# Kernel optimization log

Hardware: AMD Instinct MI355X
Metric: run time of the kernel (lower is better)

Reference implementation:

```python
import jax, jax.numpy as jnp
import numpy as np

T, B, D, H, O = 512, 64, 512, 1024, 512

def _xavier(key, shape):
    fan_out, fan_in = shape
    limit = np.sqrt(6.0 / (fan_in + fan_out))
    return jax.random.uniform(key, shape, jnp.float32, -limit, limit)

def setup_inputs() -> dict:
    key = jax.random.key(0)
    ks = jax.random.split(key, 10)
    x = jax.random.normal(ks[0], (T, B, D), jnp.float32)
    # Gate order: i, f, o, c (stacked along first axis for a fused 4H projection;
    # math identical to 8 separate Linears in the torch module, biases init to 0
    # but we randomize them slightly for a non-trivial reference).
    Wx = jnp.concatenate([_xavier(ks[1 + g], (H, D)) for g in range(4)], axis=0)  # [4H, D]
    Wh = jnp.concatenate([_xavier(ks[5 + g], (H, H)) for g in range(4)], axis=0)  # [4H, H]
    bx = jnp.zeros((4 * H,), jnp.float32)
    bh = jnp.zeros((4 * H,), jnp.float32)
    Why = _xavier(ks[9], (O, H))
    bhy = jnp.zeros((O,), jnp.float32)
    return {"x": x, "Wx": Wx, "bx": bx, "Wh": Wh, "bh": bh, "Why": Why, "bhy": bhy}

def reference(x, Wx, bx, Wh, bh, Why, bhy):
    Hd = Wh.shape[1]
    Bd = x.shape[1]
    # Precompute all input-path projections in one batched GEMM: [T, B, 4H]
    xp = jnp.einsum('tbd,gd->tbg', x, Wx) + bx + bh

    def step(carry, xp_t):
        h, c = carry
        gates = xp_t + h @ Wh.T  # [B, 4H]
        i_t = jax.nn.sigmoid(gates[:, 0 * Hd:1 * Hd])
        f_t = jax.nn.sigmoid(gates[:, 1 * Hd:2 * Hd])
        o_t = jax.nn.sigmoid(gates[:, 2 * Hd:3 * Hd])
        c_tilde = jnp.tanh(gates[:, 3 * Hd:4 * Hd])
        c = f_t * c + i_t * c_tilde
        h = o_t * jnp.tanh(c)
        return (h, c), None

    h0 = jnp.zeros((Bd, Hd), x.dtype)
    c0 = jnp.zeros((Bd, Hd), x.dtype)
    (h, c), _ = jax.lax.scan(step, (h0, c0), xp)
    return h @ Why.T + bhy  # [B, O]
```

## Files before the change

### kernel.cpp

```cpp
#include <hip/hip_runtime.h>
#include <hip/hip_bf16.h>
#include <math.h>

constexpr int T = 512;
constexpr int B = 64;
constexpr int D = 512;
constexpr int H = 1024;
constexpr int O = 512;
constexpr int GROUPS = 2;
constexpr int BG   = B / GROUPS;
constexpr int GBLK = 128;
constexpr int COLS = 32;
constexpr int KCH  = (D + H) / 8;

typedef __attribute__((ext_vector_type(8))) __bf16 bf16x8;
typedef __attribute__((ext_vector_type(4))) float  floatx4;

struct GBar {
    unsigned arr[GBLK];
};

__global__ __launch_bounds__(256) void convert_w(
    const float* __restrict__ Wx, const float* __restrict__ Wh,
    __bf16* __restrict__ Wc)
{
    const int id = blockIdx.x * 256 + threadIdx.x;
    if (id >= GBLK * KCH * COLS) return;
    const int nl     = id & 31;
    const int kchunk = (id >> 5) % KCH;
    const int strip  = id / (KCH * COLS);
    const int s  = nl >> 4;
    const int jl = (nl >> 2) & 3;
    const int g  = nl & 3;
    const int j  = strip * 8 + 2 * jl + s;
    const int k0 = kchunk * 8;
    const float* src = (k0 < D) ? &Wx[(size_t)(g * H + j) * D + k0]
                                : &Wh[(size_t)(g * H + j) * H + (k0 - D)];
    const float4 a = *(const float4*)src;
    const float4 b = *(const float4*)(src + 4);
    __bf16 t8[8] = {(__bf16)a.x,(__bf16)a.y,(__bf16)a.z,(__bf16)a.w,
                    (__bf16)b.x,(__bf16)b.y,(__bf16)b.z,(__bf16)b.w};
    *(uint4*)&Wc[(size_t)id * 8] = *(uint4*)t8;
}

__global__ __launch_bounds__(256) void make_bias(
    const float* __restrict__ bx, const float* __restrict__ bh,
    float* __restrict__ bias)
{
    const int n = blockIdx.x * 256 + threadIdx.x;
    if (n < 4 * H) {
        const int gbn = n >> 5, nl = n & 31;
        const int s  = nl >> 4;
        const int jl = (nl >> 2) & 3;
        const int g  = nl & 3;
        const int j  = gbn * 8 + 2 * jl + s;
        bias[n] = bx[g * H + j] + bh[g * H + j];
    }
}

__global__ __launch_bounds__(128, 1) void lstm_persistent(
    const float* __restrict__ x,
    const __bf16* __restrict__ Wc,
    const float* __restrict__ bias,
    __bf16* __restrict__ hbufs,
    float* __restrict__ hfin,
    GBar* bars)
{
    __shared__ __attribute__((aligned(16))) __bf16 wlds[KCH * COLS * 8];

    const int tid   = threadIdx.x;
    const int wid   = tid >> 6;
    const int lane  = tid & 63;
    const int cm    = lane & 15;
    const int q     = lane >> 4;
    const int group = blockIdx.x >> 7;
    const int gb    = blockIdx.x & 127;
    const int n0    = gb * COLS;
    GBar* bar = bars + group;
    __bf16* hb0 = hbufs + (size_t)group * 2 * BG * H;
    __bf16* hb1 = hb0 + BG * H;

    {
        const uint4* wsrc = (const uint4*)(Wc + (size_t)gb * KCH * COLS * 8);
        uint4* wdst = (uint4*)wlds;
        for (int i = tid; i < KCH * COLS; i += 128) wdst[i] = wsrc[i];
    }
    const int p4 = cm & 3;
    const int jl = cm >> 2;
    const int row_l = wid * 16 + q * 4 + p4;
    const float4 bias0q = *(const float4*)&bias[n0 + jl * 4];
    const float4 bias1q = *(const float4*)&bias[n0 + 16 + jl * 4];
    float c0 = 0.f, c1 = 0.f;
    __syncthreads();

    const int grow = group * BG + wid * 16 + cm;
    const float* xrow = x + (size_t)grow * D + q * 8;
    const int    hoff = (wid * 16 + cm) * H + q * 8;
    const __bf16* wl  = wlds + (q * 32 + cm) * 8;
    const unsigned* fa = bar->arr + (lane & 31);

    floatx4 acc[2][2];
    float4  xcur[16][2];

    auto loadx = [&](int tt) {
        const float* xr = xrow + (size_t)tt * (B * D);
        #pragma unroll
        for (int s = 0; s < 16; ++s) {
            xcur[s][0] = *(const float4*)(xr + s * 32);
            xcur[s][1] = *(const float4*)(xr + s * 32 + 4);
        }
    };
    auto xmfma = [&]() {
        acc[0][0] = (floatx4){0,0,0,0}; acc[0][1] = (floatx4){0,0,0,0};
        acc[1][0] = (floatx4){0,0,0,0}; acc[1][1] = (floatx4){0,0,0,0};
        #pragma unroll
        for (int s = 0; s < 16; ++s) {
            const float4 a0 = xcur[s][0], a1 = xcur[s][1];
            const bf16x8 af = {(__bf16)a0.x,(__bf16)a0.y,(__bf16)a0.z,(__bf16)a0.w,
                               (__bf16)a1.x,(__bf16)a1.y,(__bf16)a1.z,(__bf16)a1.w};
            const bf16x8 b0 = *(const bf16x8*)(wl + s * 1024);
            const bf16x8 b1 = *(const bf16x8*)(wl + s * 1024 + 128);
            acc[0][s & 1] = __builtin_amdgcn_mfma_f32_16x16x32_bf16(af, b0, acc[0][s & 1], 0, 0, 0);
            acc[1][s & 1] = __builtin_amdgcn_mfma_f32_16x16x32_bf16(af, b1, acc[1][s & 1], 0, 0, 0);
        }
    };

    auto quadT = [&](float v[4]) {
        float w0 = __shfl_xor(v[1], 1), w1 = __shfl_xor(v[0], 1);
        float w2 = __shfl_xor(v[3], 1), w3 = __shfl_xor(v[2], 1);
        if (p4 & 1) { v[0] = w0; v[2] = w2; } else { v[1] = w1; v[3] = w3; }
        w0 = __shfl_xor(v[2], 2); w1 = __shfl_xor(v[3], 2);
        w2 = __shfl_xor(v[0], 2); w3 = __shfl_xor(v[1], 2);
        if (p4 & 2) { v[0] = w0; v[1] = w1; } else { v[2] = w2; v[3] = w3; }
    };

    loadx(0);
    xmfma();

    for (int t = 0; t < T; ++t) {
        const __bf16* hcur = (t & 1) ? hb1 : hb0;
        __bf16*       hnxt = (t & 1) ? hb0 : hb1;

        {
            const __bf16* hbase = hcur + hoff;
            uint4 hv[32];
            unsigned ftmp;
            asm volatile(
                "1: global_load_dword %[f], %[fa], off sc0 sc1\n\t"
                "s_waitcnt vmcnt(0)\n\t"
                "v_cmp_gt_i32 vcc, %[tt], %[f]\n\t"
                "s_cbranch_vccnz 1b\n\t"
                "global_load_dwordx4 %[h0], %[hb], off sc0 sc1\n\t"
                "global_load_dwordx4 %[h1], %[hb], off offset:64 sc0 sc1\n\t"
                "global_load_dwordx4 %[h2], %[hb], off offset:128 sc0 sc1\n\t"
                "global_load_dwordx4 %[h3], %[hb], off offset:192 sc0 sc1\n\t"
                "global_load_dwordx4 %[h4], %[hb], off offset:256 sc0 sc1\n\t"
                "global_load_dwordx4 %[h5], %[hb], off offset:320 sc0 sc1\n\t"
                "global_load_dwordx4 %[h6], %[hb], off offset:384 sc0 sc1\n\t"
                "global_load_dwordx4 %[h7], %[hb], off offset:448 sc0 sc1\n\t"
                "1: global_load_dword %[f], %[fa], off offset:128 sc0 sc1\n\t"
                "s_waitcnt vmcnt(0)\n\t"
                "v_cmp_gt_i32 vcc, %[tt], %[f]\n\t"
                "s_cbranch_vccnz 1b\n\t"
                "global_load_dwordx4 %[h8], %[hb], off offset:512 sc0 sc1\n\t"
                "global_load_dwordx4 %[h9], %[hb], off offset:576 sc0 sc1\n\t"
                "global_load_dwordx4 %[h10], %[hb], off offset:640 sc0 sc1\n\t"
                "global_load_dwordx4 %[h11], %[hb], off offset:704 sc0 sc1\n\t"
                "global_load_dwordx4 %[h12], %[hb], off offset:768 sc0 sc1\n\t"
                "global_load_dwordx4 %[h13], %[hb], off offset:832 sc0 sc1\n\t"
                "global_load_dwordx4 %[h14], %[hb], off offset:896 sc0 sc1\n\t"
                "global_load_dwordx4 %[h15], %[hb], off offset:960 sc0 sc1\n\t"
                "1: global_load_dword %[f], %[fa], off offset:256 sc0 sc1\n\t"
                "s_waitcnt vmcnt(0)\n\t"
                "v_cmp_gt_i32 vcc, %[tt], %[f]\n\t"
                "s_cbranch_vccnz 1b\n\t"
                "global_load_dwordx4 %[h16], %[hb], off offset:1024 sc0 sc1\n\t"
                "global_load_dwordx4 %[h17], %[hb], off offset:1088 sc0 sc1\n\t"
                "global_load_dwordx4 %[h18], %[hb], off offset:1152 sc0 sc1\n\t"
                "global_load_dwordx4 %[h19], %[hb], off offset:1216 sc0 sc1\n\t"
                "global_load_dwordx4 %[h20], %[hb], off offset:1280 sc0 sc1\n\t"
                "global_load_dwordx4 %[h21], %[hb], off offset:1344 sc0 sc1\n\t"
                "global_load_dwordx4 %[h22], %[hb], off offset:1408 sc0 sc1\n\t"
                "global_load_dwordx4 %[h23], %[hb], off offset:1472 sc0 sc1\n\t"
                "1: global_load_dword %[f], %[fa], off offset:384 sc0 sc1\n\t"
                "s_waitcnt vmcnt(0)\n\t"
                "v_cmp_gt_i32 vcc, %[tt], %[f]\n\t"
                "s_cbranch_vccnz 1b\n\t"
                "global_load_dwordx4 %[h24], %[hb], off offset:1536 sc0 sc1\n\t"
                "global_load_dwordx4 %[h25], %[hb], off offset:1600 sc0 sc1\n\t"
                "global_load_dwordx4 %[h26], %[hb], off offset:1664 sc0 sc1\n\t"
                "global_load_dwordx4 %[h27], %[hb], off offset:1728 sc0 sc1\n\t"
                "global_load_dwordx4 %[h28], %[hb], off offset:1792 sc0 sc1\n\t"
                "global_load_dwordx4 %[h29], %[hb], off offset:1856 sc0 sc1\n\t"
                "global_load_dwordx4 %[h30], %[hb], off offset:1920 sc0 sc1\n\t"
                "global_load_dwordx4 %[h31], %[hb], off offset:1984 sc0 sc1\n\t"
                "s_waitcnt vmcnt(0)"
                : [h0]"=&v"(hv[0]),  [h1]"=&v"(hv[1]),  [h2]"=&v"(hv[2]),  [h3]"=&v"(hv[3]),
                  [h4]"=&v"(hv[4]),  [h5]"=&v"(hv[5]),  [h6]"=&v"(hv[6]),  [h7]"=&v"(hv[7]),
                  [h8]"=&v"(hv[8]),  [h9]"=&v"(hv[9]),  [h10]"=&v"(hv[10]), [h11]"=&v"(hv[11]),
                  [h12]"=&v"(hv[12]), [h13]"=&v"(hv[13]), [h14]"=&v"(hv[14]), [h15]"=&v"(hv[15]),
                  [h16]"=&v"(hv[16]), [h17]"=&v"(hv[17]), [h18]"=&v"(hv[18]), [h19]"=&v"(hv[19]),
                  [h20]"=&v"(hv[20]), [h21]"=&v"(hv[21]), [h22]"=&v"(hv[22]), [h23]"=&v"(hv[23]),
                  [h24]"=&v"(hv[24]), [h25]"=&v"(hv[25]), [h26]"=&v"(hv[26]), [h27]"=&v"(hv[27]),
                  [h28]"=&v"(hv[28]), [h29]"=&v"(hv[29]), [h30]"=&v"(hv[30]), [h31]"=&v"(hv[31]),
                  [f]"=&v"(ftmp)
                : [hb]"v"(hbase), [fa]"v"(fa), [tt]"v"(t)
                : "memory", "vcc");
            #pragma unroll
            for (int sg = 0; sg < 32; ++sg) {
                union { uint4 u; bf16x8 v; } hf; hf.u = hv[sg];
                const bf16x8 b0 = *(const bf16x8*)(wl + 16384 + sg * 1024);
                const bf16x8 b1 = *(const bf16x8*)(wl + 16384 + sg * 1024 + 128);
                acc[0][sg & 1] = __builtin_amdgcn_mfma_f32_16x16x32_bf16(hf.v, b0, acc[0][sg & 1], 0, 0, 0);
                acc[1][sg & 1] = __builtin_amdgcn_mfma_f32_16x16x32_bf16(hf.v, b1, acc[1][sg & 1], 0, 0, 0);
            }
        }
        const floatx4 av0 = acc[0][0] + acc[0][1];
        const floatx4 av1 = acc[1][0] + acc[1][1];

        float g0v[4] = {av0.x, av0.y, av0.z, av0.w};
        float g1v[4] = {av1.x, av1.y, av1.z, av1.w};
        quadT(g0v);
        quadT(g1v);

        if (t + 1 < T) loadx(t + 1);

        const float i0 = 1.f / (1.f + expf(-(g0v[0] + bias0q.x)));
        const float f0 = 1.f / (1.f + expf(-(g0v[1] + bias0q.y)));
        const float o0 = 1.f / (1.f + expf(-(g0v[2] + bias0q.z)));
        const float t0 = tanhf(g0v[3] + bias0q.w);
        const float i1 = 1.f / (1.f + expf(-(g1v[0] + bias1q.x)));
        const float f1 = 1.f / (1.f + expf(-(g1v[1] + bias1q.y)));
        const float o1 = 1.f / (1.f + expf(-(g1v[2] + bias1q.z)));
        const float t1 = tanhf(g1v[3] + bias1q.w);
        c0 = f0 * c0 + i0 * t0;
        c1 = f1 * c1 + i1 * t1;
        const float hv0 = o0 * tanhf(c0);
        const float hv1 = o1 * tanhf(c1);
        const int j0 = gb * 8 + 2 * jl;
        const int hi = row_l * H + j0;
        union { __bf16 h2[2]; unsigned u; } hp;
        hp.h2[0] = (__bf16)hv0; hp.h2[1] = (__bf16)hv1;
        __hip_atomic_store((unsigned*)&hnxt[hi], hp.u, __ATOMIC_RELAXED,
                           __HIP_MEMORY_SCOPE_AGENT);
        if (t == T - 1) {
            const int gr = group * BG + row_l;
            hfin[gr * H + j0]     = hv0;
            hfin[gr * H + j0 + 1] = hv1;
        }

        __syncthreads();

        if (tid == 0)
            __hip_atomic_store(&bar->arr[gb], (unsigned)(t + 1),
                               __ATOMIC_RELAXED, __HIP_MEMORY_SCOPE_AGENT);

        if (t + 1 < T) xmfma();
    }
}

__global__ __launch_bounds__(256) void out_gemm(
    const float* __restrict__ h, const float* __restrict__ Why,
    const float* __restrict__ bhy, float* __restrict__ out)
{
    const int idx = blockIdx.x * 256 + threadIdx.x;
    if (idx >= B * O) return;
    const int b = idx / O;
    const int o = idx % O;
    const float4* hv = (const float4*)&h[(size_t)b * H];
    const float4* wv = (const float4*)&Why[(size_t)o * H];
    float s = 0.f;
    #pragma unroll 4
    for (int k = 0; k < H / 4; ++k) {
        const float4 a = hv[k];
        const float4 w = wv[k];
        s += a.x * w.x + a.y * w.y + a.z * w.z + a.w * w.w;
    }
    out[idx] = s + bhy[o];
}

extern "C" void kernel_launch(void* const* d_in, const int* in_sizes, int n_in,
                              void* d_out, int out_size, void* d_ws, size_t ws_size,
                              hipStream_t stream) {
    const float* x   = (const float*)d_in[0];
    const float* Wx  = (const float*)d_in[1];
    const float* bx  = (const float*)d_in[2];
    const float* Wh  = (const float*)d_in[3];
    const float* bh  = (const float*)d_in[4];
    const float* Why = (const float*)d_in[5];
    const float* bhy = (const float*)d_in[6];
    float* out = (float*)d_out;

    char* ws = (char*)d_ws;
    __bf16* Wc    = (__bf16*)ws;
    float*  bias  = (float*)(ws + 12582912);
    __bf16* hbufs = (__bf16*)(ws + 12599296);
    GBar*   bars  = (GBar*)  (ws + 12861440);
    float*  hfin  = (float*)ws;

    (void)hipMemsetAsync(ws + 12599296, 0, 262144 + 2 * sizeof(GBar), stream);
    convert_w<<<3072, 256, 0, stream>>>(Wx, Wh, Wc);
    make_bias<<<16, 256, 0, stream>>>(bx, bh, bias);

    lstm_persistent<<<GROUPS * GBLK, 128, 0, stream>>>(x, Wc, bias, hbufs,
                                                       hfin, bars);

    out_gemm<<<(B * O + 255) / 256, 256, 0, stream>>>(hfin, Why, bhy, out);
}
```

Before: 3.527 ms.

## Offload grid-barrier polling to a dedicated wavefront signaling compute waves via LDS

Adds a third wavefront per block that polls the global per-block step counters and publishes per-quarter readiness flags into shared memory. It also writes this block's own counter after the per-step __syncthreads. The compute wavefronts now spin on cheap LDS reads instead of issuing global loads of the flag array, which moves global polling traffic off the critical path. The cost is an extra wave per block and an added __syncthreads handshake between the poller and compute waves each step. The poller also sleeps between polls, which can add wake-up latency.

After: 4.847 ms. +37.4%, slower.

```diff
diff --git a/kernel.cpp b/kernel.cpp
--- a/kernel.cpp
+++ b/kernel.cpp
@@ -58,7 +58,7 @@
     }
 }
 
-__global__ __launch_bounds__(128, 1) void lstm_persistent(
+__global__ __launch_bounds__(192, 1) void lstm_persistent(
     const float* __restrict__ x,
     const __bf16* __restrict__ Wc,
     const float* __restrict__ bias,
@@ -67,6 +67,7 @@
     GBar* bars)
 {
     __shared__ __attribute__((aligned(16))) __bf16 wlds[KCH * COLS * 8];
+    __shared__ int sflag[4];
 
     const int tid   = threadIdx.x;
     const int wid   = tid >> 6;
@@ -83,21 +84,48 @@
     {
         const uint4* wsrc = (const uint4*)(Wc + (size_t)gb * KCH * COLS * 8);
         uint4* wdst = (uint4*)wlds;
-        for (int i = tid; i < KCH * COLS; i += 128) wdst[i] = wsrc[i];
-    }
+        for (int i = tid; i < KCH * COLS; i += 192) wdst[i] = wsrc[i];
+    }
+    if (tid < 4) sflag[tid] = -1;
+    __syncthreads();
+
+    if (wid == 2) {
+        const unsigned* fp = bar->arr + 2 * lane;
+        for (int t = 0; t < T; ++t) {
+            const int want = t;
+            for (;;) {
+                uint2 fv;
+                asm volatile("global_load_dwordx2 %0, %1, off sc0 sc1\n\t"
+                             "s_waitcnt vmcnt(0)"
+                             : "=v"(fv) : "v"(fp) : "memory");
+                const int mn = (int)(fv.x < fv.y ? fv.x : fv.y);
+                const unsigned long long b = __ballot(mn >= want);
+                if (lane < 4 &&
+                    (((b >> (16 * lane)) & 0xFFFFull) == 0xFFFFull))
+                    ((volatile int*)sflag)[lane] = want;
+                if (b == ~0ull) break;
+                __builtin_amdgcn_s_sleep(1);
+            }
+            __syncthreads();
+            if (lane == 0)
+                __hip_atomic_store(&bar->arr[gb], (unsigned)(t + 1),
+                                   __ATOMIC_RELAXED, __HIP_MEMORY_SCOPE_AGENT);
+        }
+        return;
+    }
+
     const int p4 = cm & 3;
     const int jl = cm >> 2;
     const int row_l = wid * 16 + q * 4 + p4;
     const float4 bias0q = *(const float4*)&bias[n0 + jl * 4];
     const float4 bias1q = *(const float4*)&bias[n0 + 16 + jl * 4];
     float c0 = 0.f, c1 = 0.f;
-    __syncthreads();
 
     const int grow = group * BG + wid * 16 + cm;
     const float* xrow = x + (size_t)grow * D + q * 8;
     const int    hoff = (wid * 16 + cm) * H + q * 8;
     const __bf16* wl  = wlds + (q * 32 + cm) * 8;
-    const unsigned* fa = bar->arr + (lane & 31);
+    const unsigned sfa = (unsigned)(size_t)(&sflag[0]);
 
     floatx4 acc[2][2];
     float4  xcur[16][2];
@@ -146,8 +174,8 @@
             uint4 hv[32];
             unsigned ftmp;
             asm volatile(
-                "1: global_load_dword %[f], %[fa], off sc0 sc1\n\t"
-                "s_waitcnt vmcnt(0)\n\t"
+                "1: ds_read_b32 %[f], %[sa]\n\t"
+                "s_waitcnt lgkmcnt(0)\n\t"
                 "v_cmp_gt_i32 vcc, %[tt], %[f]\n\t"
                 "s_cbranch_vccnz 1b\n\t"
                 "global_load_dwordx4 %[h0], %[hb], off sc0 sc1\n\t"
@@ -158,8 +186,8 @@
                 "global_load_dwordx4 %[h5], %[hb], off offset:320 sc0 sc1\n\t"
                 "global_load_dwordx4 %[h6], %[hb], off offset:384 sc0 sc1\n\t"
                 "global_load_dwordx4 %[h7], %[hb], off offset:448 sc0 sc1\n\t"
-                "1: global_load_dword %[f], %[fa], off offset:128 sc0 sc1\n\t"
-                "s_waitcnt vmcnt(0)\n\t"
+                "1: ds_read_b32 %[f], %[sa] offset:4\n\t"
+                "s_waitcnt lgkmcnt(0)\n\t"
                 "v_cmp_gt_i32 vcc, %[tt], %[f]\n\t"
                 "s_cbranch_vccnz 1b\n\t"
                 "global_load_dwordx4 %[h8], %[hb], off offset:512 sc0 sc1\n\t"
@@ -170,8 +198,8 @@
                 "global_load_dwordx4 %[h13], %[hb], off offset:832 sc0 sc1\n\t"
                 "global_load_dwordx4 %[h14], %[hb], off offset:896 sc0 sc1\n\t"
                 "global_load_dwordx4 %[h15], %[hb], off offset:960 sc0 sc1\n\t"
-                "1: global_load_dword %[f], %[fa], off offset:256 sc0 sc1\n\t"
-                "s_waitcnt vmcnt(0)\n\t"
+                "1: ds_read_b32 %[f], %[sa] offset:8\n\t"
+                "s_waitcnt lgkmcnt(0)\n\t"
                 "v_cmp_gt_i32 vcc, %[tt], %[f]\n\t"
                 "s_cbranch_vccnz 1b\n\t"
                 "global_load_dwordx4 %[h16], %[hb], off offset:1024 sc0 sc1\n\t"
@@ -182,8 +210,8 @@
                 "global_load_dwordx4 %[h21], %[hb], off offset:1344 sc0 sc1\n\t"
                 "global_load_dwordx4 %[h22], %[hb], off offset:1408 sc0 sc1\n\t"
                 "global_load_dwordx4 %[h23], %[hb], off offset:1472 sc0 sc1\n\t"
-                "1: global_load_dword %[f], %[fa], off offset:384 sc0 sc1\n\t"
-                "s_waitcnt vmcnt(0)\n\t"
+                "1: ds_read_b32 %[f], %[sa] offset:12\n\t"
+                "s_waitcnt lgkmcnt(0)\n\t"
                 "v_cmp_gt_i32 vcc, %[tt], %[f]\n\t"
                 "s_cbranch_vccnz 1b\n\t"
                 "global_load_dwordx4 %[h24], %[hb], off offset:1536 sc0 sc1\n\t"
@@ -204,7 +232,7 @@
                   [h24]"=&v"(hv[24]), [h25]"=&v"(hv[25]), [h26]"=&v"(hv[26]), [h27]"=&v"(hv[27]),
                   [h28]"=&v"(hv[28]), [h29]"=&v"(hv[29]), [h30]"=&v"(hv[30]), [h31]"=&v"(hv[31]),
                   [f]"=&v"(ftmp)
-                : [hb]"v"(hbase), [fa]"v"(fa), [tt]"v"(t)
+                : [hb]"v"(hbase), [sa]"v"(sfa), [tt]"v"(t)
                 : "memory", "vcc");
             #pragma unroll
             for (int sg = 0; sg < 32; ++sg) {
@@ -251,10 +279,6 @@
 
         __syncthreads();
 
-        if (tid == 0)
-            __hip_atomic_store(&bar->arr[gb], (unsigned)(t + 1),
-                               __ATOMIC_RELAXED, __HIP_MEMORY_SCOPE_AGENT);
-
         if (t + 1 < T) xmfma();
     }
 }
@@ -302,7 +326,7 @@
     convert_w<<<3072, 256, 0, stream>>>(Wx, Wh, Wc);
     make_bias<<<16, 256, 0, stream>>>(bx, bh, bias);
 
-    lstm_persistent<<<GROUPS * GBLK, 128, 0, stream>>>(x, Wc, bias, hbufs,
+    lstm_persistent<<<GROUPS * GBLK, 192, 0, stream>>>(x, Wc, bias, hbufs,
                                                        hfin, bars);
 
     out_gemm<<<(B * O + 255) / 256, 256, 0, stream>>>(hfin, Why, bhy, out);
```
